# Optimization experiments

Hardware: AMD Instinct MI355X
Metric: run time of the kernel (lower is better)

Reference implementation:

```python
import jax, jax.numpy as jnp
import numpy as np

IN_FEATURES = 512
OUT_FEATURES = 512
GRID_SIZE = 5
SPLINE_ORDER = 3
GRID_RANGE = (-1.0, 1.0)
BATCH = 16384


def make_grid():
    h = (GRID_RANGE[1] - GRID_RANGE[0]) / GRID_SIZE
    g = jnp.arange(-SPLINE_ORDER, GRID_SIZE + SPLINE_ORDER + 1, dtype=jnp.float32) * h + GRID_RANGE[0]
    return jnp.broadcast_to(g, (IN_FEATURES, g.shape[0]))  # [in, 12]


def setup_inputs() -> dict:
    key = jax.random.key(0)
    k1, k2, k3, k4 = jax.random.split(key, 4)
    x = jax.random.normal(k1, (BATCH, IN_FEATURES), dtype=jnp.float32)
    base_weight = jax.random.normal(k2, (OUT_FEATURES, IN_FEATURES), dtype=jnp.float32) * (1.0 / np.sqrt(IN_FEATURES))
    spline_weight = jax.random.normal(k3, (OUT_FEATURES, IN_FEATURES, GRID_SIZE + SPLINE_ORDER), dtype=jnp.float32) * 0.02
    spline_scaler = jax.random.normal(k4, (OUT_FEATURES, IN_FEATURES), dtype=jnp.float32) * (1.0 / np.sqrt(IN_FEATURES))
    grid = make_grid()
    return {"x": x, "base_weight": base_weight, "spline_weight": spline_weight,
            "spline_scaler": spline_scaler, "grid": grid}


def b_splines(x, grid):
    # x: [B, in], grid: [in, G+2k+1] -> bases: [B, in, G+k]
    xe = x[:, :, None]
    bases = ((xe >= grid[:, :-1]) & (xe < grid[:, 1:])).astype(x.dtype)
    for k in range(1, SPLINE_ORDER + 1):
        left = (xe - grid[:, :-(k + 1)]) / (grid[:, k:-1] - grid[:, :-(k + 1)])
        right = (grid[:, k + 1:] - xe) / (grid[:, k + 1:] - grid[:, 1:-k])
        bases = left * bases[:, :, :-1] + right * bases[:, :, 1:]
    return bases


def reference(x, base_weight, spline_weight, spline_scaler, grid):
    B = x.shape[0]
    base_out = jax.nn.silu(x) @ base_weight.T  # [B, out]
    bases = b_splines(x, grid)  # [B, in, G+k]
    scaled_w = spline_weight * spline_scaler[:, :, None]  # [out, in, G+k]
    spline_out = bases.reshape(B, -1) @ scaled_w.reshape(OUT_FEATURES, -1).T  # [B, out]
    return base_out + spline_out
```

## Files before the change

### kernel.cpp

```cpp
#include <hip/hip_runtime.h>

typedef unsigned char u8;
typedef unsigned short u16;
typedef unsigned int u32;
typedef unsigned long long u64;
typedef __attribute__((ext_vector_type(4))) float f32x4;
typedef __attribute__((ext_vector_type(8))) float f32x8;
typedef __attribute__((ext_vector_type(4))) u16 u16x4;
typedef __attribute__((ext_vector_type(8))) u16 u16x8;
typedef __attribute__((ext_vector_type(2))) u64 u64x2;
typedef __attribute__((ext_vector_type(8))) __bf16 bf16x8;

#define IN_F 512
#define OUT_F 512
#define BM 64
#define NSPL 64
#define NSIL 8
#define WSCALE 64.0f
#define WDESCALE 0.015625f

__device__ __forceinline__ u16 f2bf(float f) {
  u32 u = __float_as_uint(f);
  return (u16)((u + 0x7FFFu + ((u >> 16) & 1u)) >> 16);
}
__device__ __forceinline__ float siluf(float v) { return v / (1.0f + __expf(-v)); }

__device__ __forceinline__ u32 cvtpk_fp8(float a, float b) {
  u32 d;
  asm("v_cvt_pk_fp8_f32 %0, %1, %2" : "=v"(d) : "v"(a), "v"(b));
  return d & 0xFFFFu;
}

__device__ __forceinline__ u64 spl8f8(float xv) {
  float u = fmaf(xv, 2.5f, 5.5f);
  float cf = floorf(u);
  float f = u - cf;
  int c = (int)cf;
  bool valid = (u >= 0.0f) && (u < 11.0f);
  c = c < 0 ? 0 : (c > 10 ? 10 : c);
  float f2 = f * f, f3 = f2 * f, v1 = 1.0f - f;
  float w0 = v1 * v1 * v1 * (1.0f / 6.0f);
  float w1 = 0.5f * f3 - f2 + (2.0f / 3.0f);
  float w2 = -0.5f * f3 + 0.5f * f2 + 0.5f * f + (1.0f / 6.0f);
  float w3 = f3 * (1.0f / 6.0f);
  u32 lo = cvtpk_fp8(w0, w1), hi = cvtpk_fp8(w2, w3);
  u64 W = ((u64)(lo | (hi << 16))) << 24;
  int sh = (6 - c) * 8;
  u64 r = (sh >= 0) ? (W >> sh) : (W << (-sh));
  return valid ? r : 0ull;
}

__global__ __launch_bounds__(256) void kan_prep(const float* __restrict__ bw,
                                                const float* __restrict__ sw,
                                                const float* __restrict__ ss,
                                                u8* __restrict__ Wf8,
                                                u16* __restrict__ Wf16) {
  __shared__ u8 PL[17152];
  const int tid = threadIdx.x;
  const int b = blockIdx.x;
  if (b < 128) {
    const int og = b & 31, ib = b >> 5;
    const int o_loc = tid >> 4, seg = tid & 15;
    const int orow = og * 16 + o_loc;
    const float* swp = sw + ((size_t)orow * 512 + ib * 128) * 8 + seg * 64;
    const float* ssp = ss + (size_t)orow * 512 + ib * 128;
    u8* L8 = PL;
#pragma unroll
    for (int q = 0; q < 16; ++q) {
      f32x4 v = *(const f32x4*)(swp + q * 4);
      const int el = seg * 64 + q * 4;
      float sv = ssp[el >> 3] * WSCALE;
      u32 lo = cvtpk_fp8(v[0] * sv, v[1] * sv);
      u32 hi = cvtpk_fp8(v[2] * sv, v[3] * sv);
      *(u32*)&L8[o_loc * 1048 + el] = lo | (hi << 16);
    }
    __syncthreads();
    const int s16 = tid & 31;
    const int o15a = (s16 * 2) & 15, lkv = (s16 * 2) >> 4;
#pragma unroll
    for (int cp = 0; cp < 4; ++cp) {
      const int stq_loc = cp * 8 + (tid >> 5);
      const int i_loc = stq_loc * 4 + lkv;
      u64 d0 = *(const u64*)&L8[o15a * 1048 + i_loc * 8];
      u64 d1 = *(const u64*)&L8[(o15a + 1) * 1048 + i_loc * 8];
      u64x2 dd = {d0, d1};
      *(u64x2*)&Wf8[(size_t)((ib * 32 + stq_loc) * 32 + og) * 512 + s16 * 16] = dd;
    }
  } else {
    const int og = b - 128;
    u16* L16 = (u16*)PL;
#pragma unroll
    for (int p = 0; p < 8; ++p) {
      const int flat = tid * 4 + p * 1024;
      const int o_loc = flat >> 9, k = flat & 511;
      f32x4 v = *(const f32x4*)(bw + (size_t)(og * 16 + o_loc) * 512 + k);
      u16x4 h;
#pragma unroll
      for (int e = 0; e < 4; ++e) h[e] = f2bf(v[e]);
      *(u16x4*)&L16[o_loc * 536 + k] = h;
    }
    __syncthreads();
    const int s = tid & 63;
    const int o15 = s & 15, g3 = s >> 4;
#pragma unroll
    for (int cp = 0; cp < 4; ++cp) {
      const int gq = cp * 4 + (tid >> 6);
      u16x8 d = *(const u16x8*)&L16[o15 * 536 + (gq * 4 + g3) * 8];
      *(u16x8*)&Wf16[(size_t)(gq * 32 + og) * 512 + s * 8] = d;
    }
  }
}

__global__ __launch_bounds__(256, 2) void kan_gemm(const float* __restrict__ x,
                                                   const u8* __restrict__ Wf8,
                                                   const u16* __restrict__ Wf16,
                                                   float* __restrict__ out) {
  __shared__ u16 As16[2][4096];
  __shared__ u8 As8[2][4096];
  const int tid = threadIdx.x;
  const int b = blockIdx.x;
  const int nh = (b >> 2) & 1;
  const int n0 = nh * 256;
  const int m0 = ((b & 3) | ((b >> 3) << 2)) * BM;

  const int lane = tid & 63;
  const int wv = tid >> 6;
  const int lr = lane & 15;
  const int lk = lane >> 4;

  const u8* b8base = Wf8 + (size_t)(nh * 16 + wv * 4) * 512 + lane * 8;
  const u16* b16base = Wf16 + (size_t)(nh * 16 + wv * 4) * 512 + lane * 8;

  const int oct = tid & 7, rr = tid >> 3;
  const float* xr0 = x + (size_t)(m0 + rr) * IN_F;
  const float* xr1 = xr0 + (size_t)32 * IN_F;
  const int woff = rr * 64 + (oct ^ (rr & 7)) * 8;
  const int ro0 = lr * 64 + (lk ^ (lr & 7)) * 8;
  const int ro1 = lr * 64 + ((4 + lk) ^ (lr & 7)) * 8;

  f32x4 acc[4][4];
  const f32x4 zero = {0.0f, 0.0f, 0.0f, 0.0f};
#pragma unroll
  for (int m = 0; m < 4; ++m)
#pragma unroll
    for (int n = 0; n < 4; ++n) acc[m][n] = zero;

  u64 b8A[8], b8B[8];
  bf16x8 brA16[8], brB16[8];
  float xpA0, xpA1, xpB0, xpB1;
  f32x8 xsA0, xsA1, xsB0, xsB1;

#define BAR()                                              \
  {                                                        \
    asm volatile("s_waitcnt lgkmcnt(0)" ::: "memory");     \
    __builtin_amdgcn_s_barrier();                          \
  }

#define LOADB8(REG, ST)                                                        \
  {                                                                            \
    const u8* p_ = b8base + (size_t)(ST)*32768;                                \
    _Pragma("unroll") for (int s_ = 0; s_ < 2; ++s_)                           \
      _Pragma("unroll") for (int n_ = 0; n_ < 4; ++n_)                         \
        REG[s_ * 4 + n_] = *(const u64*)(p_ + s_ * 16384 + n_ * 512);          \
  }

#define LOADB16(REG, KT)                                                       \
  {                                                                            \
    const u16* p_ = b16base + (size_t)(KT)*32768;                              \
    _Pragma("unroll") for (int s_ = 0; s_ < 2; ++s_)                           \
      _Pragma("unroll") for (int n_ = 0; n_ < 4; ++n_)                         \
        REG[s_ * 4 + n_] = *(const bf16x8*)(p_ + s_ * 16384 + n_ * 512);       \
  }

#define APRE_SPL(X0, X1, ST)                                                   \
  {                                                                            \
    X0 = xr0[(ST)*8 + oct];                                                    \
    X1 = xr1[(ST)*8 + oct];                                                    \
  }

#define AWRITE_SPL(BUF, X0, X1)                                                \
  {                                                                            \
    *(u64*)&As8[BUF][woff] = spl8f8(X0);                                       \
    *(u64*)&As8[BUF][woff + 2048] = spl8f8(X1);                                \
  }

#define APRE_SIL(XS0, XS1, KT)                                                 \
  {                                                                            \
    XS0 = *(const f32x8*)(xr0 + (KT)*64 + oct * 8);                            \
    XS1 = *(const f32x8*)(xr1 + (KT)*64 + oct * 8);                            \
  }

#define AWRITE_SIL(BUF, XS0, XS1)                                              \
  {                                                                            \
    u16x8 p0_, p1_;                                                            \
    _Pragma("unroll") for (int e_ = 0; e_ < 8; ++e_) {                         \
      p0_[e_] = f2bf(siluf(XS0[e_]));                                          \
      p1_[e_] = f2bf(siluf(XS1[e_]));                                          \
    }                                                                          \
    *(u16x8*)&As16[BUF][woff] = p0_;                                           \
    *(u16x8*)&As16[BUF][woff + 2048] = p1_;                                    \
  }

#define READ8(AF, BUF, RO)                                                     \
  _Pragma("unroll") for (int m_ = 0; m_ < 4; ++m_)                             \
      AF[m_] = *(const u64*)&As8[BUF][(RO) + m_ * 1024];

#define READ16(AF, BUF, RO)                                                    \
  _Pragma("unroll") for (int m_ = 0; m_ < 4; ++m_)                             \
      AF[m_] = *(const bf16x8*)&As16[BUF][(RO) + m_ * 1024];

#define MFMA8(AF, BREG, SB)                                                    \
  __builtin_amdgcn_s_setprio(1);                                               \
  _Pragma("unroll") for (int m_ = 0; m_ < 4; ++m_)                             \
    _Pragma("unroll") for (int n_ = 0; n_ < 4; ++n_)                           \
      acc[m_][n_] = __builtin_amdgcn_mfma_f32_16x16x32_fp8_fp8(                \
          (long)AF[m_], (long)BREG[(SB) + n_], acc[m_][n_], 0, 0, 0);          \
  __builtin_amdgcn_s_setprio(0);

#define MFMA16(AF, BREG, SB)                                                   \
  __builtin_amdgcn_s_setprio(1);                                               \
  _Pragma("unroll") for (int m_ = 0; m_ < 4; ++m_)                             \
    _Pragma("unroll") for (int n_ = 0; n_ < 4; ++n_)                           \
      acc[m_][n_] = __builtin_amdgcn_mfma_f32_16x16x32_bf16(                   \
          AF[m_], BREG[(SB) + n_], acc[m_][n_], 0, 0, 0);                      \
  __builtin_amdgcn_s_setprio(0);

  APRE_SPL(xpA0, xpA1, 0);
  LOADB8(b8A, 0);
  AWRITE_SPL(0, xpA0, xpA1);
  APRE_SPL(xpB0, xpB1, 1);
  BAR();

  for (int st = 0; st < NSPL; st += 2) {
    {
      u64 af0[4], af1[4];
      LOADB8(b8B, st + 1);
      READ8(af0, 0, ro0);
      AWRITE_SPL(1, xpB0, xpB1);
      if (st + 2 < NSPL) { APRE_SPL(xpA0, xpA1, st + 2); }
      MFMA8(af0, b8A, 0);
      READ8(af1, 0, ro1);
      MFMA8(af1, b8A, 4);
    }
    BAR();
    {
      u64 af0[4], af1[4];
      if (st + 2 < NSPL) { LOADB8(b8A, st + 2); }
      else { LOADB16(brA16, 0); }
      READ8(af0, 1, ro0);
      if (st + 2 < NSPL) { AWRITE_SPL(0, xpA0, xpA1); }
      if (st + 3 < NSPL) { APRE_SPL(xpB0, xpB1, st + 3); }
      else if (st + 2 >= NSPL) { APRE_SIL(xsA0, xsA1, 0); }
      MFMA8(af0, b8B, 0);
      READ8(af1, 1, ro1);
      MFMA8(af1, b8B, 4);
    }
    BAR();
  }

  AWRITE_SIL(0, xsA0, xsA1);
  APRE_SIL(xsB0, xsB1, 1);
#pragma unroll
  for (int m = 0; m < 4; ++m)
#pragma unroll
    for (int n = 0; n < 4; ++n) acc[m][n] *= WDESCALE;
  BAR();

#define SIL_PHASE(KT, CB, CBREG, NBREG, SRC0, SRC1, TGT0, TGT1)                \
  {                                                                            \
    bf16x8 af0[4], af1[4];                                                     \
    if ((KT) < 7) { LOADB16(NBREG, (KT) + 1); }                                \
    READ16(af0, CB, ro0);                                                      \
    if ((KT) < 7) { AWRITE_SIL(((KT) + 1) & 1, SRC0, SRC1); }                  \
    if ((KT) < 6) { APRE_SIL(TGT0, TGT1, (KT) + 2); }                          \
    MFMA16(af0, CBREG, 0);                                                     \
    READ16(af1, CB, ro1);                                                      \
    MFMA16(af1, CBREG, 4);                                                     \
    if ((KT) < 7) BAR();                                                       \
  }

  SIL_PHASE(0, 0, brA16, brB16, xsB0, xsB1, xsA0, xsA1);
  SIL_PHASE(1, 1, brB16, brA16, xsA0, xsA1, xsB0, xsB1);
  SIL_PHASE(2, 0, brA16, brB16, xsB0, xsB1, xsA0, xsA1);
  SIL_PHASE(3, 1, brB16, brA16, xsA0, xsA1, xsB0, xsB1);
  SIL_PHASE(4, 0, brA16, brB16, xsB0, xsB1, xsA0, xsA1);
  SIL_PHASE(5, 1, brB16, brA16, xsA0, xsA1, xsB0, xsB1);
  SIL_PHASE(6, 0, brA16, brB16, xsB0, xsB1, xsA0, xsA1);
  SIL_PHASE(7, 1, brB16, brA16, xsA0, xsA1, xsB0, xsB1);

#pragma unroll
  for (int m = 0; m < 4; ++m)
#pragma unroll
    for (int n = 0; n < 4; ++n)
#pragma unroll
      for (int j = 0; j < 4; ++j)
        out[(size_t)(m0 + m * 16 + lk * 4 + j) * OUT_F + n0 + wv * 64 + n * 16 + lr] =
            acc[m][n][j];

#undef BAR
#undef LOADB8
#undef LOADB16
#undef APRE_SPL
#undef AWRITE_SPL
#undef APRE_SIL
#undef AWRITE_SIL
#undef READ8
#undef READ16
#undef MFMA8
#undef MFMA16
#undef SIL_PHASE
}

extern "C" void kernel_launch(void* const* d_in, const int* in_sizes, int n_in,
                              void* d_out, int out_size, void* d_ws, size_t ws_size,
                              hipStream_t stream) {
  const float* x  = (const float*)d_in[0];
  const float* bw = (const float*)d_in[1];
  const float* sw = (const float*)d_in[2];
  const float* ss = (const float*)d_in[3];
  u8* Wf8 = (u8*)d_ws;
  u16* Wf16 = (u16*)((u8*)d_ws + (2u << 20));

  kan_prep<<<dim3(160), 256, 0, stream>>>(bw, sw, ss, Wf8, Wf16);
  kan_gemm<<<dim3(512), 256, 0, stream>>>(x, Wf8, Wf16, (float*)d_out);
}
```

Measured before the change: 168.1 us.

## Switch to 32x32 scaled FP8 MFMA and 32x32 bf16 MFMA with relaid weights

The spline GEMM now uses the MI355 scaled f8f6f4 32x32x64 MFMA instead of 16x16x32 fp8. The scale operands fold in the 1/64 weight descale, so the explicit accumulator rescale is dropped. The silu GEMM moves to 32x32x16 bf16 MFMA. Weight prep and the LDS layouts (padded 40-byte rows for fp8 A) are rewritten so each lane loads contiguous 32-byte B fragments. The goal is fewer MFMA issues and fewer LDS reads per FLOP, at the cost of a different register footprint and new bank-conflict behaviour.

```diff
diff --git a/kernel.cpp b/kernel.cpp
--- a/kernel.cpp
+++ b/kernel.cpp
@@ -6,18 +6,16 @@
 typedef unsigned long long u64;
 typedef __attribute__((ext_vector_type(4))) float f32x4;
 typedef __attribute__((ext_vector_type(8))) float f32x8;
-typedef __attribute__((ext_vector_type(4))) u16 u16x4;
+typedef __attribute__((ext_vector_type(16))) float f32x16;
+typedef __attribute__((ext_vector_type(8))) int i32x8;
+typedef __attribute__((ext_vector_type(4))) u32 u32x4;
 typedef __attribute__((ext_vector_type(8))) u16 u16x8;
-typedef __attribute__((ext_vector_type(2))) u64 u64x2;
 typedef __attribute__((ext_vector_type(8))) __bf16 bf16x8;
 
-#define IN_F 512
-#define OUT_F 512
-#define BM 64
 #define NSPL 64
-#define NSIL 8
-#define WSCALE 64.0f
-#define WDESCALE 0.015625f
+#define NSILST 8
+#define SCL_A 0x7F7F7F7F
+#define SCL_B 0x79797979
 
 __device__ __forceinline__ u16 f2bf(float f) {
   u32 u = __float_as_uint(f);
@@ -54,140 +52,119 @@
                                                 const float* __restrict__ sw,
                                                 const float* __restrict__ ss,
                                                 u8* __restrict__ Wf8,
-                                                u16* __restrict__ Wf16) {
-  __shared__ u8 PL[17152];
-  const int tid = threadIdx.x;
-  const int b = blockIdx.x;
-  if (b < 128) {
-    const int og = b & 31, ib = b >> 5;
-    const int o_loc = tid >> 4, seg = tid & 15;
-    const int orow = og * 16 + o_loc;
-    const float* swp = sw + ((size_t)orow * 512 + ib * 128) * 8 + seg * 64;
-    const float* ssp = ss + (size_t)orow * 512 + ib * 128;
-    u8* L8 = PL;
-#pragma unroll
-    for (int q = 0; q < 16; ++q) {
-      f32x4 v = *(const f32x4*)(swp + q * 4);
-      const int el = seg * 64 + q * 4;
-      float sv = ssp[el >> 3] * WSCALE;
-      u32 lo = cvtpk_fp8(v[0] * sv, v[1] * sv);
-      u32 hi = cvtpk_fp8(v[2] * sv, v[3] * sv);
-      *(u32*)&L8[o_loc * 1048 + el] = lo | (hi << 16);
+                                                u16* __restrict__ Wf16b) {
+  const int tid = threadIdx.x, b = blockIdx.x;
+  const int l = tid & 63;
+  if (b < 256) {
+    const int chunk = b * 4 + (tid >> 6);
+    const int kt = chunk >> 4, nt = chunk & 15;
+    const int o = nt * 32 + (l & 31);
+    const int kbase = kt * 64 + (l >> 5) * 32;
+    const float* swp = sw + (size_t)o * 4096 + kbase;
+    f32x4 sv4 = *(const f32x4*)(ss + (size_t)o * 512 + (kbase >> 3));
+    u32 w[8];
+#pragma unroll
+    for (int q = 0; q < 4; ++q) {
+      float s = sv4[q] * 64.0f;
+      f32x8 f = *(const f32x8*)(swp + q * 8);
+      w[q * 2]     = cvtpk_fp8(f[0] * s, f[1] * s) | (cvtpk_fp8(f[2] * s, f[3] * s) << 16);
+      w[q * 2 + 1] = cvtpk_fp8(f[4] * s, f[5] * s) | (cvtpk_fp8(f[6] * s, f[7] * s) << 16);
     }
-    __syncthreads();
-    const int s16 = tid & 31;
-    const int o15a = (s16 * 2) & 15, lkv = (s16 * 2) >> 4;
-#pragma unroll
-    for (int cp = 0; cp < 4; ++cp) {
-      const int stq_loc = cp * 8 + (tid >> 5);
-      const int i_loc = stq_loc * 4 + lkv;
-      u64 d0 = *(const u64*)&L8[o15a * 1048 + i_loc * 8];
-      u64 d1 = *(const u64*)&L8[(o15a + 1) * 1048 + i_loc * 8];
-      u64x2 dd = {d0, d1};
-      *(u64x2*)&Wf8[(size_t)((ib * 32 + stq_loc) * 32 + og) * 512 + s16 * 16] = dd;
-    }
+    u32* dst = (u32*)(Wf8 + (size_t)chunk * 2048 + l * 32);
+    u32x4 d0 = {w[0], w[1], w[2], w[3]};
+    u32x4 d1 = {w[4], w[5], w[6], w[7]};
+    *(u32x4*)dst = d0;
+    *(u32x4*)(dst + 4) = d1;
   } else {
-    const int og = b - 128;
-    u16* L16 = (u16*)PL;
-#pragma unroll
-    for (int p = 0; p < 8; ++p) {
-      const int flat = tid * 4 + p * 1024;
-      const int o_loc = flat >> 9, k = flat & 511;
-      f32x4 v = *(const f32x4*)(bw + (size_t)(og * 16 + o_loc) * 512 + k);
-      u16x4 h;
-#pragma unroll
-      for (int e = 0; e < 4; ++e) h[e] = f2bf(v[e]);
-      *(u16x4*)&L16[o_loc * 536 + k] = h;
-    }
-    __syncthreads();
-    const int s = tid & 63;
-    const int o15 = s & 15, g3 = s >> 4;
-#pragma unroll
-    for (int cp = 0; cp < 4; ++cp) {
-      const int gq = cp * 4 + (tid >> 6);
-      u16x8 d = *(const u16x8*)&L16[o15 * 536 + (gq * 4 + g3) * 8];
-      *(u16x8*)&Wf16[(size_t)(gq * 32 + og) * 512 + s * 8] = d;
-    }
+    const int chunk = (b - 256) * 4 + (tid >> 6);
+    const int ks = chunk >> 4, nt = chunk & 15;
+    const int o = nt * 32 + (l & 31);
+    const int k0 = ks * 16 + (l >> 5) * 8;
+    f32x8 f = *(const f32x8*)(bw + (size_t)o * 512 + k0);
+    u16x8 h;
+#pragma unroll
+    for (int e = 0; e < 8; ++e) h[e] = f2bf(f[e]);
+    *(u16x8*)(Wf16b + (size_t)chunk * 512 + l * 8) = h;
   }
 }
 
 __global__ __launch_bounds__(256, 2) void kan_gemm(const float* __restrict__ x,
                                                    const u8* __restrict__ Wf8,
-                                                   const u16* __restrict__ Wf16,
+                                                   const u16* __restrict__ Wf16b,
                                                    float* __restrict__ out) {
+  __shared__ u8 As8[2][5120];
   __shared__ u16 As16[2][4096];
-  __shared__ u8 As8[2][4096];
   const int tid = threadIdx.x;
   const int b = blockIdx.x;
   const int nh = (b >> 2) & 1;
   const int n0 = nh * 256;
-  const int m0 = ((b & 3) | ((b >> 3) << 2)) * BM;
+  const int m0 = ((b & 3) | ((b >> 3) << 2)) * 64;
 
   const int lane = tid & 63;
   const int wv = tid >> 6;
-  const int lr = lane & 15;
-  const int lk = lane >> 4;
-
-  const u8* b8base = Wf8 + (size_t)(nh * 16 + wv * 4) * 512 + lane * 8;
-  const u16* b16base = Wf16 + (size_t)(nh * 16 + wv * 4) * 512 + lane * 8;
-
-  const int oct = tid & 7, rr = tid >> 3;
-  const float* xr0 = x + (size_t)(m0 + rr) * IN_F;
-  const float* xr1 = xr0 + (size_t)32 * IN_F;
-  const int woff = rr * 64 + (oct ^ (rr & 7)) * 8;
-  const int ro0 = lr * 64 + (lk ^ (lr & 7)) * 8;
-  const int ro1 = lr * 64 + ((4 + lk) ^ (lr & 7)) * 8;
-
-  f32x4 acc[4][4];
-  const f32x4 zero = {0.0f, 0.0f, 0.0f, 0.0f};
-#pragma unroll
-  for (int m = 0; m < 4; ++m)
-#pragma unroll
-    for (int n = 0; n < 4; ++n) acc[m][n] = zero;
-
-  u64 b8A[8], b8B[8];
+  const int r5 = lane & 31;
+  const int kh = lane >> 5;
+
+  const int ntbase = nh * 8 + wv * 2;
+  const u8* b8base = Wf8 + (size_t)ntbase * 2048 + lane * 32;
+  const u16* b16base = Wf16b + (size_t)ntbase * 512 + lane * 8;
+
+  const int sr = tid & 63;
+  const int sq = tid >> 6;
+  const float* xrow = x + (size_t)(m0 + sr) * 512;
+  const int c0 = sq * 2;
+  const int w8off = ((sr >> 5) * 2 + (c0 >> 2)) * 1280 + (sr & 31) * 40 + (c0 & 3) * 8;
+  const int w16off = ((sr >> 5) * 8 + sq * 2) * 256 + (sr & 31) * 8;
+
+  f32x16 acc[2][2];
+  const f32x16 z16 = {0.f,0.f,0.f,0.f,0.f,0.f,0.f,0.f,0.f,0.f,0.f,0.f,0.f,0.f,0.f,0.f};
+#pragma unroll
+  for (int mt = 0; mt < 2; ++mt)
+#pragma unroll
+    for (int nt = 0; nt < 2; ++nt) acc[mt][nt] = z16;
+
+  i32x8 b8A[2], b8B[2];
   bf16x8 brA16[8], brB16[8];
   float xpA0, xpA1, xpB0, xpB1;
   f32x8 xsA0, xsA1, xsB0, xsB1;
 
-#define BAR()                                              \
-  {                                                        \
-    asm volatile("s_waitcnt lgkmcnt(0)" ::: "memory");     \
-    __builtin_amdgcn_s_barrier();                          \
-  }
-
-#define LOADB8(REG, ST)                                                        \
-  {                                                                            \
-    const u8* p_ = b8base + (size_t)(ST)*32768;                                \
-    _Pragma("unroll") for (int s_ = 0; s_ < 2; ++s_)                           \
-      _Pragma("unroll") for (int n_ = 0; n_ < 4; ++n_)                         \
-        REG[s_ * 4 + n_] = *(const u64*)(p_ + s_ * 16384 + n_ * 512);          \
-  }
-
-#define LOADB16(REG, KT)                                                       \
-  {                                                                            \
-    const u16* p_ = b16base + (size_t)(KT)*32768;                              \
-    _Pragma("unroll") for (int s_ = 0; s_ < 2; ++s_)                           \
-      _Pragma("unroll") for (int n_ = 0; n_ < 4; ++n_)                         \
-        REG[s_ * 4 + n_] = *(const bf16x8*)(p_ + s_ * 16384 + n_ * 512);       \
-  }
-
-#define APRE_SPL(X0, X1, ST)                                                   \
-  {                                                                            \
-    X0 = xr0[(ST)*8 + oct];                                                    \
-    X1 = xr1[(ST)*8 + oct];                                                    \
+#define BAR()                                            \
+  {                                                      \
+    asm volatile("s_waitcnt lgkmcnt(0)" ::: "memory");   \
+    __builtin_amdgcn_s_barrier();                        \
+  }
+
+#define LOADB8(REG, KT)                                                        \
+  {                                                                            \
+    const u8* p_ = b8base + (size_t)(KT)*32768;                                \
+    REG[0] = *(const i32x8*)p_;                                                \
+    REG[1] = *(const i32x8*)(p_ + 2048);                                       \
+  }
+
+#define LOADB16(REG, STEP)                                                     \
+  {                                                                            \
+    const u16* p_ = b16base + (size_t)(STEP)*32768;                            \
+    _Pragma("unroll") for (int ks_ = 0; ks_ < 4; ++ks_)                        \
+      _Pragma("unroll") for (int nt_ = 0; nt_ < 2; ++nt_)                      \
+        REG[ks_ * 2 + nt_] = *(const bf16x8*)(p_ + ks_ * 8192 + nt_ * 512);    \
+  }
+
+#define APRE_SPL(X0, X1, KT)                                                   \
+  {                                                                            \
+    X0 = xrow[(KT)*8 + c0];                                                    \
+    X1 = xrow[(KT)*8 + c0 + 1];                                                \
   }
 
 #define AWRITE_SPL(BUF, X0, X1)                                                \
   {                                                                            \
-    *(u64*)&As8[BUF][woff] = spl8f8(X0);                                       \
-    *(u64*)&As8[BUF][woff + 2048] = spl8f8(X1);                                \
-  }
-
-#define APRE_SIL(XS0, XS1, KT)                                                 \
-  {                                                                            \
-    XS0 = *(const f32x8*)(xr0 + (KT)*64 + oct * 8);                            \
-    XS1 = *(const f32x8*)(xr1 + (KT)*64 + oct * 8);                            \
+    *(u64*)&As8[BUF][w8off] = spl8f8(X0);                                      \
+    *(u64*)&As8[BUF][w8off + 8] = spl8f8(X1);                                  \
+  }
+
+#define APRE_SIL(XS0, XS1, STEP)                                               \
+  {                                                                            \
+    XS0 = *(const f32x8*)(xrow + (STEP)*64 + sq * 16);                         \
+    XS1 = *(const f32x8*)(xrow + (STEP)*64 + sq * 16 + 8);                     \
   }
 
 #define AWRITE_SIL(BUF, XS0, XS1)                                              \
@@ -197,33 +174,38 @@
       p0_[e_] = f2bf(siluf(XS0[e_]));                                          \
       p1_[e_] = f2bf(siluf(XS1[e_]));                                          \
     }                                                                          \
-    *(u16x8*)&As16[BUF][woff] = p0_;                                           \
-    *(u16x8*)&As16[BUF][woff + 2048] = p1_;                                    \
-  }
-
-#define READ8(AF, BUF, RO)                                                     \
-  _Pragma("unroll") for (int m_ = 0; m_ < 4; ++m_)                             \
-      AF[m_] = *(const u64*)&As8[BUF][(RO) + m_ * 1024];
-
-#define READ16(AF, BUF, RO)                                                    \
-  _Pragma("unroll") for (int m_ = 0; m_ < 4; ++m_)                             \
-      AF[m_] = *(const bf16x8*)&As16[BUF][(RO) + m_ * 1024];
-
-#define MFMA8(AF, BREG, SB)                                                    \
+    *(u16x8*)&As16[BUF][w16off] = p0_;                                         \
+    *(u16x8*)&As16[BUF][w16off + 256] = p1_;                                   \
+  }
+
+#define READA8(AF, BUF)                                                        \
+  _Pragma("unroll") for (int mt_ = 0; mt_ < 2; ++mt_) {                        \
+    const int ba_ = (mt_ * 2 + kh) * 1280 + r5 * 40;                           \
+    union { u64 q[4]; i32x8 v; } uu_;                                          \
+    uu_.q[0] = *(const u64*)&As8[BUF][ba_];                                    \
+    uu_.q[1] = *(const u64*)&As8[BUF][ba_ + 8];                                \
+    uu_.q[2] = *(const u64*)&As8[BUF][ba_ + 16];                               \
+    uu_.q[3] = *(const u64*)&As8[BUF][ba_ + 24];                               \
+    AF[mt_] = uu_.v;                                                           \
+  }
+
+#define MFMA_SPL(AF, BREG)                                                     \
   __builtin_amdgcn_s_setprio(1);                                               \
-  _Pragma("unroll") for (int m_ = 0; m_ < 4; ++m_)                             \
-    _Pragma("unroll") for (int n_ = 0; n_ < 4; ++n_)                           \
-      acc[m_][n_] = __builtin_amdgcn_mfma_f32_16x16x32_fp8_fp8(                \
-          (long)AF[m_], (long)BREG[(SB) + n_], acc[m_][n_], 0, 0, 0);          \
+  _Pragma("unroll") for (int mt_ = 0; mt_ < 2; ++mt_)                          \
+    _Pragma("unroll") for (int nt_ = 0; nt_ < 2; ++nt_)                        \
+      acc[mt_][nt_] = __builtin_amdgcn_mfma_scale_f32_32x32x64_f8f6f4(         \
+          AF[mt_], BREG[nt_], acc[mt_][nt_], 0, 0, 0, SCL_A, 0, SCL_B);        \
   __builtin_amdgcn_s_setprio(0);
 
-#define MFMA16(AF, BREG, SB)                                                   \
-  __builtin_amdgcn_s_setprio(1);                                               \
-  _Pragma("unroll") for (int m_ = 0; m_ < 4; ++m_)                             \
-    _Pragma("unroll") for (int n_ = 0; n_ < 4; ++n_)                           \
-      acc[m_][n_] = __builtin_amdgcn_mfma_f32_16x16x32_bf16(                   \
-          AF[m_], BREG[(SB) + n_], acc[m_][n_], 0, 0, 0);                      \
-  __builtin_amdgcn_s_setprio(0);
+#define READ16(AF, BUF, KS)                                                    \
+  _Pragma("unroll") for (int mt_ = 0; mt_ < 2; ++mt_)                          \
+    AF[mt_] = *(const bf16x8*)&As16[BUF][(mt_ * 8 + (KS)*2 + kh) * 256 + r5 * 8];
+
+#define MFMA_SIL(AF, BREG, KS)                                                 \
+  _Pragma("unroll") for (int mt_ = 0; mt_ < 2; ++mt_)                          \
+    _Pragma("unroll") for (int nt_ = 0; nt_ < 2; ++nt_)                        \
+      acc[mt_][nt_] = __builtin_amdgcn_mfma_f32_32x32x16_bf16(                 \
+          AF[mt_], BREG[(KS)*2 + nt_], acc[mt_][nt_], 0, 0, 0);
 
   APRE_SPL(xpA0, xpA1, 0);
   LOADB8(b8A, 0);
@@ -231,52 +213,46 @@
   APRE_SPL(xpB0, xpB1, 1);
   BAR();
 
-  for (int st = 0; st < NSPL; st += 2) {
+  for (int kt = 0; kt < NSPL; kt += 2) {
     {
-      u64 af0[4], af1[4];
-      LOADB8(b8B, st + 1);
-      READ8(af0, 0, ro0);
+      i32x8 af[2];
+      LOADB8(b8B, kt + 1);
+      READA8(af, 0);
       AWRITE_SPL(1, xpB0, xpB1);
-      if (st + 2 < NSPL) { APRE_SPL(xpA0, xpA1, st + 2); }
-      MFMA8(af0, b8A, 0);
-      READ8(af1, 0, ro1);
-      MFMA8(af1, b8A, 4);
+      if (kt + 2 < NSPL) { APRE_SPL(xpA0, xpA1, kt + 2); }
+      MFMA_SPL(af, b8A);
     }
     BAR();
     {
-      u64 af0[4], af1[4];
-      if (st + 2 < NSPL) { LOADB8(b8A, st + 2); }
+      i32x8 af[2];
+      if (kt + 2 < NSPL) { LOADB8(b8A, kt + 2); }
       else { LOADB16(brA16, 0); }
-      READ8(af0, 1, ro0);
-      if (st + 2 < NSPL) { AWRITE_SPL(0, xpA0, xpA1); }
-      if (st + 3 < NSPL) { APRE_SPL(xpB0, xpB1, st + 3); }
-      else if (st + 2 >= NSPL) { APRE_SIL(xsA0, xsA1, 0); }
-      MFMA8(af0, b8B, 0);
-      READ8(af1, 1, ro1);
-      MFMA8(af1, b8B, 4);
+      READA8(af, 1);
+      if (kt + 2 < NSPL) { AWRITE_SPL(0, xpA0, xpA1); }
+      if (kt + 3 < NSPL) { APRE_SPL(xpB0, xpB1, kt + 3); }
+      else if (kt + 2 >= NSPL) { APRE_SIL(xsA0, xsA1, 0); }
+      MFMA_SPL(af, b8B);
     }
     BAR();
   }
 
   AWRITE_SIL(0, xsA0, xsA1);
   APRE_SIL(xsB0, xsB1, 1);
-#pragma unroll
-  for (int m = 0; m < 4; ++m)
-#pragma unroll
-    for (int n = 0; n < 4; ++n) acc[m][n] *= WDESCALE;
   BAR();
 
-#define SIL_PHASE(KT, CB, CBREG, NBREG, SRC0, SRC1, TGT0, TGT1)                \
-  {                                                                            \
-    bf16x8 af0[4], af1[4];                                                     \
-    if ((KT) < 7) { LOADB16(NBREG, (KT) + 1); }                                \
-    READ16(af0, CB, ro0);                                                      \
-    if ((KT) < 7) { AWRITE_SIL(((KT) + 1) & 1, SRC0, SRC1); }                  \
-    if ((KT) < 6) { APRE_SIL(TGT0, TGT1, (KT) + 2); }                          \
-    MFMA16(af0, CBREG, 0);                                                     \
-    READ16(af1, CB, ro1);                                                      \
-    MFMA16(af1, CBREG, 4);                                                     \
-    if ((KT) < 7) BAR();                                                       \
+#define SIL_PHASE(STEP, CB, CBREG, NBREG, SRC0, SRC1, TGT0, TGT1)              \
+  {                                                                            \
+    if ((STEP) < 7) { LOADB16(NBREG, (STEP) + 1); }                            \
+    if ((STEP) < 7) { AWRITE_SIL(((STEP) + 1) & 1, SRC0, SRC1); }              \
+    if ((STEP) < 6) { APRE_SIL(TGT0, TGT1, (STEP) + 2); }                      \
+    __builtin_amdgcn_s_setprio(1);                                             \
+    _Pragma("unroll") for (int ks_ = 0; ks_ < 4; ++ks_) {                      \
+      bf16x8 af_[2];                                                           \
+      READ16(af_, CB, ks_);                                                    \
+      MFMA_SIL(af_, CBREG, ks_);                                               \
+    }                                                                          \
+    __builtin_amdgcn_s_setprio(0);                                             \
+    if ((STEP) < 7) BAR();                                                     \
   }
 
   SIL_PHASE(0, 0, brA16, brB16, xsB0, xsB1, xsA0, xsA1);
@@ -289,13 +265,15 @@
   SIL_PHASE(7, 1, brB16, brA16, xsA0, xsA1, xsB0, xsB1);
 
 #pragma unroll
-  for (int m = 0; m < 4; ++m)
-#pragma unroll
-    for (int n = 0; n < 4; ++n)
-#pragma unroll
-      for (int j = 0; j < 4; ++j)
-        out[(size_t)(m0 + m * 16 + lk * 4 + j) * OUT_F + n0 + wv * 64 + n * 16 + lr] =
-            acc[m][n][j];
+  for (int mt = 0; mt < 2; ++mt)
+#pragma unroll
+    for (int nt = 0; nt < 2; ++nt)
+#pragma unroll
+      for (int j = 0; j < 16; ++j) {
+        const int row = m0 + mt * 32 + (j & 3) + ((j >> 2) << 3) + (kh << 2);
+        const int col = n0 + wv * 64 + nt * 32 + r5;
+        out[(size_t)row * 512 + col] = acc[mt][nt][j];
+      }
 
 #undef BAR
 #undef LOADB8
@@ -304,10 +282,10 @@
 #undef AWRITE_SPL
 #undef APRE_SIL
 #undef AWRITE_SIL
-#undef READ8
+#undef READA8
+#undef MFMA_SPL
 #undef READ16
-#undef MFMA8
-#undef MFMA16
+#undef MFMA_SIL
 #undef SIL_PHASE
 }
 
@@ -319,8 +297,8 @@
   const float* sw = (const float*)d_in[2];
   const float* ss = (const float*)d_in[3];
   u8* Wf8 = (u8*)d_ws;
-  u16* Wf16 = (u16*)((u8*)d_ws + (2u << 20));
-
-  kan_prep<<<dim3(160), 256, 0, stream>>>(bw, sw, ss, Wf8, Wf16);
-  kan_gemm<<<dim3(512), 256, 0, stream>>>(x, Wf8, Wf16, (float*)d_out);
-}
+  u16* Wf16b = (u16*)((u8*)d_ws + (2u << 20));
+
+  kan_prep<<<dim3(384), 256, 0, stream>>>(bw, sw, ss, Wf8, Wf16b);
+  kan_gemm<<<dim3(512), 256, 0, stream>>>(x, Wf8, Wf16b, (float*)d_out);
+}
```

After: 162.1 us. 1.04x faster.
